# Performance work log

Hardware: AMD Instinct MI355X
Metric: run time of the kernel (lower is better)

The kernel has to match this reference:

```python
import jax, jax.numpy as jnp
import numpy as np

EMBED_DIM = 1024
NUM_HEADS = 16
HEAD_DIM = EMBED_DIM // NUM_HEADS
SCALING = HEAD_DIM ** -0.5


def setup_inputs() -> dict:
    key = jax.random.key(0)
    ks = jax.random.split(key, 11)
    B, S, E = 4, 2048, EMBED_DIM
    s = 1.0 / np.sqrt(E)
    return {
        "query": jax.random.normal(ks[0], (B, S, E), jnp.float32),
        "key": jax.random.normal(ks[1], (B, S, E), jnp.float32),
        "value": jax.random.normal(ks[2], (B, S, E), jnp.float32),
        "q_w": jax.random.normal(ks[3], (E, E), jnp.float32) * s,
        "q_b": jax.random.normal(ks[4], (E,), jnp.float32) * 0.01,
        "k_w": jax.random.normal(ks[5], (E, E), jnp.float32) * s,
        "k_b": jax.random.normal(ks[6], (E,), jnp.float32) * 0.01,
        "v_w": jax.random.normal(ks[7], (E, E), jnp.float32) * s,
        "v_b": jax.random.normal(ks[8], (E,), jnp.float32) * 0.01,
        "out_w": jax.random.normal(ks[9], (E, E), jnp.float32) * s,
        "out_b": jax.random.normal(ks[10], (E,), jnp.float32) * 0.01,
    }


def reference(query, key, value, q_w, q_b, k_w, k_b, v_w, v_b, out_w, out_b):
    B, S, E = query.shape
    H, D = NUM_HEADS, HEAD_DIM
    # torch Linear: x @ W.T + b
    q = (query @ q_w.T + q_b).reshape(B, S, H, D).transpose(0, 2, 1, 3)  # [B,H,S,D]
    k = (key @ k_w.T + k_b).reshape(B, -1, H, D).transpose(0, 2, 1, 3)
    v = (value @ v_w.T + v_b).reshape(B, -1, H, D).transpose(0, 2, 1, 3)
    attn_scores = jnp.einsum("bhsd,bhtd->bhst", q, k) * SCALING  # [B,H,S,S]
    attn_weights = jax.nn.softmax(attn_scores, axis=-1)
    attn_output = jnp.einsum("bhst,bhtd->bhsd", attn_weights, v)
    attn_output = attn_output.transpose(0, 2, 1, 3).reshape(B, S, E)
    return attn_output @ out_w.T + out_b
```

## Files before the change

### kernel.cpp

```cpp
#include <hip/hip_runtime.h>
#include <stdint.h>
#include <stddef.h>

#define BB 4
#define SS 2048
#define EE 1024
#define HH 16
#define DD 64
#define MTOT (BB * SS)

#define SOFTMAX_C (0.125f * 1.44269504088896340736f)

using bf16x8 = __attribute__((ext_vector_type(8))) __bf16;
using f32x4  = __attribute__((ext_vector_type(4))) float;
using s16x4  = __attribute__((ext_vector_type(4))) short;

__device__ inline unsigned short f2bf(float f) {
    union { float f; uint32_t u; } v; v.f = f;
    uint32_t u = v.u;
    u += 0x7fffu + ((u >> 16) & 1u);
    return (unsigned short)(u >> 16);
}

__device__ inline uint32_t packbf_trunc(float lo, float hi) {
    union { float f; uint32_t u; } a, b; a.f = lo; b.f = hi;
    return (a.u >> 16) | (b.u & 0xFFFF0000u);
}

__device__ inline void gld_lds16(const unsigned short* g, unsigned short* l) {
    __builtin_amdgcn_global_load_lds(
        (const __attribute__((address_space(1))) unsigned int*)g,
        (__attribute__((address_space(3))) unsigned int*)l,
        16, 0, 0);
}

__global__ __launch_bounds__(256) void cast3_f32_bf16(
    const float* __restrict__ a, const float* __restrict__ b,
    const float* __restrict__ c,
    unsigned short* __restrict__ oa, unsigned short* __restrict__ ob,
    unsigned short* __restrict__ oc, int n4) {
    int i = blockIdx.x * 256 + threadIdx.x;
    const float* src = (blockIdx.y == 0) ? a : (blockIdx.y == 1) ? b : c;
    unsigned short* dst = (blockIdx.y == 0) ? oa : (blockIdx.y == 1) ? ob : oc;
    if (i < n4) {
        float4 f = ((const float4*)src)[i];
        ushort4 o;
        o.x = f2bf(f.x); o.y = f2bf(f.y); o.z = f2bf(f.z); o.w = f2bf(f.w);
        ((ushort4*)dst)[i] = o;
    }
}

__global__ __launch_bounds__(256) void cast4_f32_bf16(
    const float* __restrict__ a, const float* __restrict__ b,
    const float* __restrict__ c, const float* __restrict__ d,
    unsigned short* __restrict__ oa, unsigned short* __restrict__ ob,
    unsigned short* __restrict__ oc, unsigned short* __restrict__ od, int n4) {
    int i = blockIdx.x * 256 + threadIdx.x;
    const float* src = (blockIdx.y == 0) ? a : (blockIdx.y == 1) ? b
                     : (blockIdx.y == 2) ? c : d;
    unsigned short* dst = (blockIdx.y == 0) ? oa : (blockIdx.y == 1) ? ob
                        : (blockIdx.y == 2) ? oc : od;
    if (i < n4) {
        float4 f = ((const float4*)src)[i];
        ushort4 o;
        o.x = f2bf(f.x); o.y = f2bf(f.y); o.z = f2bf(f.z); o.w = f2bf(f.w);
        ((ushort4*)dst)[i] = o;
    }
}

template <int MODE>
__global__ __launch_bounds__(256) void gemm_nt(
    const unsigned short* __restrict__ A,
    const unsigned short* __restrict__ W,
    const float* __restrict__ bias,
    void* __restrict__ outp, float oscale) {
    __shared__ __align__(16) unsigned short As[128 * 64];
    __shared__ __align__(16) unsigned short Bs[128 * 64];

    const int tid  = threadIdx.x;
    const int lane = tid & 63;
    const int wid  = tid >> 6;
    const int wm   = wid >> 1;
    const int wn   = wid & 1;
    const int quad = lane >> 4;
    const int l16  = lane & 15;
    const int m0   = blockIdx.y * 128;
    const int n0   = blockIdx.x * 128;

    f32x4 acc[4][4];
#pragma unroll
    for (int i = 0; i < 4; i++)
#pragma unroll
        for (int j = 0; j < 4; j++) acc[i][j] = (f32x4){0.f, 0.f, 0.f, 0.f};

    const int lrow = lane >> 3;
    const int lcol = (lane & 7) * 8;
    const unsigned short* ga = A + (size_t)(m0 + wid * 32 + lrow) * 1024 + lcol;
    const unsigned short* gb = W + (size_t)(n0 + wid * 32 + lrow) * 1024 + lcol;
    unsigned short* la = As + wid * 32 * 64;
    unsigned short* lb = Bs + wid * 32 * 64;

    for (int k0 = 0; k0 < 1024; k0 += 64) {
        __syncthreads();
#pragma unroll
        for (int c = 0; c < 4; c++) {
            gld_lds16(ga + (size_t)c * 8 * 1024 + k0, la + c * 8 * 64);
            gld_lds16(gb + (size_t)c * 8 * 1024 + k0, lb + c * 8 * 64);
        }
        __syncthreads();

#pragma unroll
        for (int kt = 0; kt < 2; kt++) {
            bf16x8 a[4], b[4];
#pragma unroll
            for (int mt = 0; mt < 4; mt++)
                a[mt] = *(const bf16x8*)(As + (wm * 64 + mt * 16 + l16) * 64 + kt * 32 + quad * 8);
#pragma unroll
            for (int nt = 0; nt < 4; nt++)
                b[nt] = *(const bf16x8*)(Bs + (wn * 64 + nt * 16 + l16) * 64 + kt * 32 + quad * 8);
#pragma unroll
            for (int mt = 0; mt < 4; mt++)
#pragma unroll
                for (int nt = 0; nt < 4; nt++)
                    acc[mt][nt] = __builtin_amdgcn_mfma_f32_16x16x32_bf16(
                        a[mt], b[nt], acc[mt][nt], 0, 0, 0);
        }
    }

#pragma unroll
    for (int mt = 0; mt < 4; mt++) {
#pragma unroll
        for (int nt = 0; nt < 4; nt++) {
            int gcol = n0 + wn * 64 + nt * 16 + l16;
            float bvn = (MODE != 3) ? bias[gcol] : 0.f;
#pragma unroll
            for (int r = 0; r < 4; r++) {
                int grow = m0 + wm * 64 + mt * 16 + quad * 4 + r;
                float bv = (MODE == 3) ? bias[grow] : bvn;
                float v = (acc[mt][nt][r] + bv) * oscale;
                if (MODE == 0) {
                    int bb = grow >> 11, sr = grow & 2047;
                    int hh = gcol >> 6,  dd = gcol & 63;
                    ((unsigned short*)outp)[(((size_t)(bb * HH + hh)) * SS + sr) * DD + dd] = f2bf(v);
                } else if (MODE == 3) {
                    int bb = gcol >> 11, sr = gcol & 2047;
                    int hh = grow >> 6,  dd = grow & 63;
                    ((unsigned short*)outp)[(((size_t)(bb * HH + hh)) * DD + dd) * SS + sr] = f2bf(v);
                } else {
                    ((float*)outp)[(size_t)grow * 1024 + gcol] = v;
                }
            }
        }
    }
}

__global__ __launch_bounds__(256) void flash_attn5(
    const unsigned short* __restrict__ Qh,
    const unsigned short* __restrict__ Kh,
    const unsigned short* __restrict__ Vtg,
    unsigned short* __restrict__ attn) {
    constexpr int LS = 72;
    __shared__ __align__(16) unsigned short Sh[128 * LS];
    unsigned short* Ks = Sh;
    unsigned short* Vs = Sh + 64 * LS;

    const int tid  = threadIdx.x;
    const int lane = tid & 63;
    const int w    = tid >> 6;
    const int quad = lane >> 4;
    const int l16  = lane & 15;
    const int bh   = blockIdx.y;
    const int q0   = blockIdx.x * 128;
    const size_t base = (size_t)bh * SS * DD;

    union { unsigned short u[4]; s16x4 v; } onesu;
#pragma unroll
    for (int i = 0; i < 4; i++) onesu.u[i] = 0x3F80;
    const s16x4 ones = onesu.v;

    bf16x8 bq[2][2];
#pragma unroll
    for (int s = 0; s < 2; s++)
#pragma unroll
        for (int kt = 0; kt < 2; kt++)
            bq[s][kt] = *(const bf16x8*)(Qh + base +
                (size_t)(q0 + w * 32 + s * 16 + l16) * DD + kt * 32 + quad * 8);

    f32x4 oT[2][4];
    f32x4 lacc[2];
#pragma unroll
    for (int s = 0; s < 2; s++) {
        lacc[s] = (f32x4){0.f, 0.f, 0.f, 0.f};
#pragma unroll
        for (int dt = 0; dt < 4; dt++) oT[s][dt] = (f32x4){0.f, 0.f, 0.f, 0.f};
    }

    for (int j0 = 0; j0 < SS; j0 += 64) {
        __syncthreads();
#pragma unroll
        for (int i = 0; i < 2; i++) {
            int c = tid + 256 * i;
            int row = c >> 3, col8 = (c & 7) * 8;
            *(uint4*)(Ks + row * LS + col8) =
                *(const uint4*)(Kh + base + (size_t)(j0 + row) * DD + col8);
            *(uint4*)(Vs + row * LS + col8) =
                *(const uint4*)(Vtg + base + (size_t)row * SS + j0 + col8);
        }
        __syncthreads();

        f32x4 sacc[2][4];
#pragma unroll
        for (int s = 0; s < 2; s++)
#pragma unroll
            for (int mt = 0; mt < 4; mt++) sacc[s][mt] = (f32x4){0.f, 0.f, 0.f, 0.f};
#pragma unroll
        for (int kt = 0; kt < 2; kt++) {
            bf16x8 ak[4];
#pragma unroll
            for (int mt = 0; mt < 4; mt++)
                ak[mt] = *(const bf16x8*)(Ks + (mt * 16 + l16) * LS + kt * 32 + quad * 8);
#pragma unroll
            for (int s = 0; s < 2; s++)
#pragma unroll
                for (int mt = 0; mt < 4; mt++)
                    sacc[s][mt] = __builtin_amdgcn_mfma_f32_16x16x32_bf16(
                        ak[mt], bq[s][kt], sacc[s][mt], 0, 0, 0);
        }

        s16x4 bpf[2][4];
#pragma unroll
        for (int s = 0; s < 2; s++) {
#pragma unroll
            for (int mt = 0; mt < 4; mt++) {
                float p0 = __builtin_amdgcn_exp2f(sacc[s][mt][0]);
                float p1 = __builtin_amdgcn_exp2f(sacc[s][mt][1]);
                float p2 = __builtin_amdgcn_exp2f(sacc[s][mt][2]);
                float p3 = __builtin_amdgcn_exp2f(sacc[s][mt][3]);
                union { uint32_t w[2]; s16x4 v; } pk;
                pk.w[0] = packbf_trunc(p0, p1);
                pk.w[1] = packbf_trunc(p2, p3);
                bpf[s][mt] = pk.v;
                lacc[s] = __builtin_amdgcn_mfma_f32_16x16x16bf16_1k(
                    ones, pk.v, lacc[s], 0, 0, 0);
            }
        }

#pragma unroll
        for (int mt = 0; mt < 4; mt++) {
#pragma unroll
            for (int dt = 0; dt < 4; dt++) {
                s16x4 av = *(const s16x4*)(Vs + (dt * 16 + l16) * LS + mt * 16 + quad * 4);
#pragma unroll
                for (int s = 0; s < 2; s++)
                    oT[s][dt] = __builtin_amdgcn_mfma_f32_16x16x16bf16_1k(
                        av, bpf[s][mt], oT[s][dt], 0, 0, 0);
            }
        }
    }

    float inv_l[2];
#pragma unroll
    for (int s = 0; s < 2; s++) inv_l[s] = 1.f / lacc[s][0];

    __syncthreads();
#pragma unroll
    for (int s = 0; s < 2; s++)
#pragma unroll
        for (int dt = 0; dt < 4; dt++)
#pragma unroll
            for (int r = 0; r < 4; r++)
                Sh[(w * 32 + s * 16 + l16) * LS + dt * 16 + quad * 4 + r] =
                    f2bf(oT[s][dt][r] * inv_l[s]);
    __syncthreads();

    const int b = bh >> 4, h = bh & 15;
#pragma unroll
    for (int i = 0; i < 4; i++) {
        int c = tid + 256 * i;
        int row = c >> 3, col8 = (c & 7) * 8;
        *(uint4*)(attn + ((size_t)b * SS + q0 + row) * EE + h * 64 + col8) =
            *(const uint4*)(Sh + row * LS + col8);
    }
}

extern "C" void kernel_launch(void* const* d_in, const int* in_sizes, int n_in,
                              void* d_out, int out_size, void* d_ws, size_t ws_size,
                              hipStream_t stream) {
    (void)in_sizes; (void)n_in; (void)out_size; (void)ws_size;
    const float* q_in  = (const float*)d_in[0];
    const float* k_in  = (const float*)d_in[1];
    const float* v_in  = (const float*)d_in[2];
    const float* q_w   = (const float*)d_in[3];
    const float* q_b   = (const float*)d_in[4];
    const float* k_w   = (const float*)d_in[5];
    const float* k_b   = (const float*)d_in[6];
    const float* v_w   = (const float*)d_in[7];
    const float* v_b   = (const float*)d_in[8];
    const float* out_w = (const float*)d_in[9];
    const float* out_b = (const float*)d_in[10];

    const size_t NX = (size_t)MTOT * EE;
    const size_t NW = (size_t)EE * EE;

    unsigned short* xq = (unsigned short*)d_ws;
    unsigned short* xk = xq + NX;
    unsigned short* xv = xk + NX;
    unsigned short* wq = xv + NX;
    unsigned short* wk = wq + NW;
    unsigned short* wv = wk + NW;
    unsigned short* wo = wv + NW;
    unsigned short* qh = wo + NW;
    unsigned short* kh = qh + NX;
    unsigned short* vt = kh + NX;
    unsigned short* attn = vt + NX;

    cast3_f32_bf16<<<dim3((int)(NX / 4 / 256), 3), 256, 0, stream>>>(
        q_in, k_in, v_in, xq, xk, xv, (int)(NX / 4));
    cast4_f32_bf16<<<dim3((int)(NW / 4 / 256), 4), 256, 0, stream>>>(
        q_w, k_w, v_w, out_w, wq, wk, wv, wo, (int)(NW / 4));

    dim3 ggrid(EE / 128, MTOT / 128);
    dim3 ggridT(MTOT / 128, EE / 128);
    gemm_nt<0><<<ggrid, 256, 0, stream>>>(xq, wq, q_b, qh, SOFTMAX_C);
    gemm_nt<0><<<ggrid, 256, 0, stream>>>(xk, wk, k_b, kh, 1.0f);
    gemm_nt<3><<<ggridT, 256, 0, stream>>>(wv, xv, v_b, vt, 1.0f);

    flash_attn5<<<dim3(SS / 128, BB * HH), 256, 0, stream>>>(qh, kh, vt, attn);

    gemm_nt<1><<<ggrid, 256, 0, stream>>>(attn, wo, out_b, (float*)d_out, 1.0f);
}
```

Baseline: 412.6 us.

## Double-buffer LDS tiles in GEMM and flash attention to overlap loads

Both the projection GEMM and the flash-attention kernel now use two LDS buffers. The next K-tile (or K/V tile) is prefetched while the current one is computed, and each iteration needs one barrier instead of two. In GEMM the direct global-to-LDS loads are issued into the alternate buffer; in attention the next tile is held in registers and written to LDS after compute. This doubles LDS use per block, which may reduce occupancy, and the attention prefetch adds register pressure.

After: 421.0 us. +2.0%, slower.

```diff
diff --git a/kernel.cpp b/kernel.cpp
--- a/kernel.cpp
+++ b/kernel.cpp
@@ -74,8 +74,8 @@
     const unsigned short* __restrict__ W,
     const float* __restrict__ bias,
     void* __restrict__ outp, float oscale) {
-    __shared__ __align__(16) unsigned short As[128 * 64];
-    __shared__ __align__(16) unsigned short Bs[128 * 64];
+    __shared__ __align__(16) unsigned short As[2][128 * 64];
+    __shared__ __align__(16) unsigned short Bs[2][128 * 64];
 
     const int tid  = threadIdx.x;
     const int lane = tid & 63;
@@ -97,27 +97,33 @@
     const int lcol = (lane & 7) * 8;
     const unsigned short* ga = A + (size_t)(m0 + wid * 32 + lrow) * 1024 + lcol;
     const unsigned short* gb = W + (size_t)(n0 + wid * 32 + lrow) * 1024 + lcol;
-    unsigned short* la = As + wid * 32 * 64;
-    unsigned short* lb = Bs + wid * 32 * 64;
-
-    for (int k0 = 0; k0 < 1024; k0 += 64) {
-        __syncthreads();
+
+    auto stage = [&](int buf, int k0) {
+        unsigned short* la = &As[buf][wid * 32 * 64];
+        unsigned short* lb = &Bs[buf][wid * 32 * 64];
 #pragma unroll
         for (int c = 0; c < 4; c++) {
             gld_lds16(ga + (size_t)c * 8 * 1024 + k0, la + c * 8 * 64);
             gld_lds16(gb + (size_t)c * 8 * 1024 + k0, lb + c * 8 * 64);
         }
-        __syncthreads();
+    };
+
+    stage(0, 0);
+    __syncthreads();
+
+    for (int k0 = 0; k0 < 1024; k0 += 64) {
+        const int cur = (k0 >> 6) & 1;
+        if (k0 + 64 < 1024) stage(cur ^ 1, k0 + 64);
 
 #pragma unroll
         for (int kt = 0; kt < 2; kt++) {
             bf16x8 a[4], b[4];
 #pragma unroll
             for (int mt = 0; mt < 4; mt++)
-                a[mt] = *(const bf16x8*)(As + (wm * 64 + mt * 16 + l16) * 64 + kt * 32 + quad * 8);
+                a[mt] = *(const bf16x8*)(&As[cur][(wm * 64 + mt * 16 + l16) * 64 + kt * 32 + quad * 8]);
 #pragma unroll
             for (int nt = 0; nt < 4; nt++)
-                b[nt] = *(const bf16x8*)(Bs + (wn * 64 + nt * 16 + l16) * 64 + kt * 32 + quad * 8);
+                b[nt] = *(const bf16x8*)(&Bs[cur][(wn * 64 + nt * 16 + l16) * 64 + kt * 32 + quad * 8]);
 #pragma unroll
             for (int mt = 0; mt < 4; mt++)
 #pragma unroll
@@ -125,6 +131,7 @@
                     acc[mt][nt] = __builtin_amdgcn_mfma_f32_16x16x32_bf16(
                         a[mt], b[nt], acc[mt][nt], 0, 0, 0);
         }
+        __syncthreads();
     }
 
 #pragma unroll
@@ -154,15 +161,13 @@
     }
 }
 
-__global__ __launch_bounds__(256) void flash_attn5(
+__global__ __launch_bounds__(256) void flash_attn6(
     const unsigned short* __restrict__ Qh,
     const unsigned short* __restrict__ Kh,
     const unsigned short* __restrict__ Vtg,
     unsigned short* __restrict__ attn) {
     constexpr int LS = 72;
-    __shared__ __align__(16) unsigned short Sh[128 * LS];
-    unsigned short* Ks = Sh;
-    unsigned short* Vs = Sh + 64 * LS;
+    __shared__ __align__(16) unsigned short KV[2][2][64 * LS];
 
     const int tid  = threadIdx.x;
     const int lane = tid & 63;
@@ -195,18 +200,36 @@
         for (int dt = 0; dt < 4; dt++) oT[s][dt] = (f32x4){0.f, 0.f, 0.f, 0.f};
     }
 
-    for (int j0 = 0; j0 < SS; j0 += 64) {
-        __syncthreads();
+    uint4 kr[2], vr[2];
+    auto load_tile = [&](int j0) {
 #pragma unroll
         for (int i = 0; i < 2; i++) {
             int c = tid + 256 * i;
             int row = c >> 3, col8 = (c & 7) * 8;
-            *(uint4*)(Ks + row * LS + col8) =
-                *(const uint4*)(Kh + base + (size_t)(j0 + row) * DD + col8);
-            *(uint4*)(Vs + row * LS + col8) =
-                *(const uint4*)(Vtg + base + (size_t)row * SS + j0 + col8);
-        }
-        __syncthreads();
+            kr[i] = *(const uint4*)(Kh + base + (size_t)(j0 + row) * DD + col8);
+            vr[i] = *(const uint4*)(Vtg + base + (size_t)row * SS + j0 + col8);
+        }
+    };
+    auto store_tile = [&](int buf) {
+#pragma unroll
+        for (int i = 0; i < 2; i++) {
+            int c = tid + 256 * i;
+            int row = c >> 3, col8 = (c & 7) * 8;
+            *(uint4*)(&KV[buf][0][row * LS + col8]) = kr[i];
+            *(uint4*)(&KV[buf][1][row * LS + col8]) = vr[i];
+        }
+    };
+
+    load_tile(0);
+    store_tile(0);
+    __syncthreads();
+
+    for (int j0 = 0; j0 < SS; j0 += 64) {
+        const int cur = (j0 >> 6) & 1;
+        const bool more = (j0 + 64) < SS;
+        if (more) load_tile(j0 + 64);
+        const unsigned short* Ks = KV[cur][0];
+        const unsigned short* Vs = KV[cur][1];
 
         f32x4 sacc[2][4];
 #pragma unroll
@@ -256,13 +279,16 @@
                         av, bpf[s][mt], oT[s][dt], 0, 0, 0);
             }
         }
+
+        if (more) store_tile(cur ^ 1);
+        __syncthreads();
     }
 
     float inv_l[2];
 #pragma unroll
     for (int s = 0; s < 2; s++) inv_l[s] = 1.f / lacc[s][0];
 
-    __syncthreads();
+    unsigned short* Sh = &KV[0][0][0];
 #pragma unroll
     for (int s = 0; s < 2; s++)
 #pragma unroll
@@ -325,7 +351,7 @@
     gemm_nt<0><<<ggrid, 256, 0, stream>>>(xk, wk, k_b, kh, 1.0f);
     gemm_nt<3><<<ggridT, 256, 0, stream>>>(wv, xv, v_b, vt, 1.0f);
 
-    flash_attn5<<<dim3(SS / 128, BB * HH), 256, 0, stream>>>(qh, kh, vt, attn);
+    flash_attn6<<<dim3(SS / 128, BB * HH), 256, 0, stream>>>(qh, kh, vt, attn);
 
     gemm_nt<1><<<ggrid, 256, 0, stream>>>(attn, wo, out_b, (float*)d_out, 1.0f);
 }
```
